# Kernel tuning notes

Measured on AMD Instinct MI355X. Metric: run time of the kernel, lower is better.

Reference implementation:

```python
import jax, jax.numpy as jnp
import numpy as np

D_MODEL = 1024
N_HEAD = 16
DK = D_MODEL // N_HEAD
D_FF = 2048
EPS = 1e-6
NEG = -1e10


def layer_norm(x, gamma, beta):
    # torch .std() is unbiased (N-1), and eps is added to std (not var)
    mean = jnp.mean(x, axis=-1, keepdims=True)
    var = jnp.sum((x - mean) ** 2, axis=-1, keepdims=True) / (x.shape[-1] - 1)
    std = jnp.sqrt(var)
    return gamma * (x - mean) / (std + EPS) + beta


def setup_inputs() -> dict:
    key = jax.random.key(0)
    ks = jax.random.split(key, 12)
    s = 0.02
    inp = {
        'x': jax.random.normal(ks[0], (16, 512, D_MODEL), dtype=jnp.float32),
        'x_mask': jax.random.randint(ks[1], (16, 1, 1, 512), 0, 2, dtype=jnp.int32),
        'Wq': jax.random.normal(ks[2], (D_MODEL, D_MODEL), dtype=jnp.float32) * s,
        'bq': jnp.zeros((D_MODEL,), jnp.float32),
        'Wk': jax.random.normal(ks[3], (D_MODEL, D_MODEL), dtype=jnp.float32) * s,
        'bk': jnp.zeros((D_MODEL,), jnp.float32),
        'Wv': jax.random.normal(ks[4], (D_MODEL, D_MODEL), dtype=jnp.float32) * s,
        'bv': jnp.zeros((D_MODEL,), jnp.float32),
        'Wo': jax.random.normal(ks[5], (D_MODEL, D_MODEL), dtype=jnp.float32) * s,
        'bo': jnp.zeros((D_MODEL,), jnp.float32),
        'gamma1': jnp.ones((D_MODEL,), jnp.float32),
        'beta1': jnp.zeros((D_MODEL,), jnp.float32),
        'W1': jax.random.normal(ks[6], (D_MODEL, D_FF), dtype=jnp.float32) * s,
        'b1': jnp.zeros((D_FF,), jnp.float32),
        'W2': jax.random.normal(ks[7], (D_FF, D_MODEL), dtype=jnp.float32) * s,
        'b2': jnp.zeros((D_MODEL,), jnp.float32),
        'gamma2': jnp.ones((D_MODEL,), jnp.float32),
        'beta2': jnp.zeros((D_MODEL,), jnp.float32),
    }
    return inp


def reference(x, x_mask, Wq, bq, Wk, bk, Wv, bv, Wo, bo, gamma1, beta1,
              W1, b1, W2, b2, gamma2, beta2):
    B, S, _ = x.shape
    # QKV projections -> [B, S, H, DK]
    q = (x @ Wq + bq).reshape(B, S, N_HEAD, DK)
    k = (x @ Wk + bk).reshape(B, S, N_HEAD, DK)
    v = (x @ Wv + bv).reshape(B, S, N_HEAD, DK)
    # scores [B, H, Sq, Sk]
    scores = jnp.einsum('bqhd,bkhd->bhqk', q, k) / jnp.sqrt(jnp.float32(DK))
    scores = jnp.where(x_mask == 0, jnp.float32(NEG), scores)
    probs = jax.nn.softmax(scores, axis=-1)
    attn = jnp.einsum('bhqk,bkhd->bqhd', probs, v).reshape(B, S, D_MODEL)
    attn_out = attn @ Wo + bo
    # residual + post-LN 1
    h = layer_norm(attn_out + x, gamma1, beta1)
    # FFN (exact GELU as torch nn.GELU default)
    ffn = jax.nn.gelu(h @ W1 + b1, approximate=False) @ W2 + b2
    out = layer_norm(ffn + h, gamma2, beta2)
    return out
```

## Files before the change

### kernel.cpp

```cpp
#include <hip/hip_runtime.h>
#include <math.h>

#define B_ 16
#define S_ 512
#define DM 1024
#define NH 16
#define DFF 2048

typedef short bf16x8 __attribute__((ext_vector_type(8)));
typedef float f32x4 __attribute__((ext_vector_type(4)));
typedef unsigned short u16;

__device__ __forceinline__ u16 f2bf(float f) {
  unsigned int u = __float_as_uint(f);
  u += 0x7FFF + ((u >> 16) & 1);
  return (u16)(u >> 16);
}

__device__ __forceinline__ float gelu_exact(float x) {
  return 0.5f * x * (1.0f + erff(x * 0.70710678118654752f));
}

__device__ __forceinline__ void gload_lds16(const void* g, void* l) {
  __builtin_amdgcn_global_load_lds((const __attribute__((address_space(1))) void*)g,
                                   (__attribute__((address_space(3))) void*)l, 16, 0, 0);
}


__global__ void cvt_bf16_k(const float* __restrict__ in, u16* __restrict__ out, int n) {
  int i = (blockIdx.x * blockDim.x + threadIdx.x) * 4;
  float4 v = *(const float4*)(in + i);
  uint2 pk;
  pk.x = (unsigned)f2bf(v.x) | ((unsigned)f2bf(v.y) << 16);
  pk.y = (unsigned)f2bf(v.z) | ((unsigned)f2bf(v.w) << 16);
  *(uint2*)(out + i) = pk;
}

__global__ void transpose_bf16(const float* __restrict__ W, u16* __restrict__ Wt, int K, int N) {
  __shared__ float tile[32][33];
  int n0 = blockIdx.x * 32, k0 = blockIdx.y * 32;
  int tx = threadIdx.x, ty = threadIdx.y;
#pragma unroll
  for (int j = 0; j < 32; j += 8)
    tile[ty + j][tx] = W[(size_t)(k0 + ty + j) * N + n0 + tx];
  __syncthreads();
#pragma unroll
  for (int j = 0; j < 32; j += 8)
    Wt[(size_t)(n0 + ty + j) * K + k0 + tx] = f2bf(tile[tx][ty + j]);
}

__global__ void bias_cat(const float* __restrict__ bq, const float* __restrict__ bk,
                         const float* __restrict__ bv, float* __restrict__ o) {
  int i = blockIdx.x * 256 + threadIdx.x;
  o[i] = (i < 1024) ? bq[i] : ((i < 2048) ? bk[i - 1024] : bv[i - 2048]);
}

template <int EPI>
__global__ __launch_bounds__(256, 3)
void gemm128(const u16* __restrict__ A, const u16* __restrict__ Bt,
             const float* __restrict__ bias, void* __restrict__ Cout,
             u16* __restrict__ vT, int M, int N, int K) {
  __shared__ __align__(16) char lds[65536];
  const int tid = threadIdx.x;
  const int w = tid >> 6, lane = tid & 63;
  const int wm = w >> 1, wn = w & 1;

  const int gx = gridDim.x;
  const int nwg = gx * gridDim.y;
  const int lin = blockIdx.y * gx + blockIdx.x;
  const int wg = (lin & 7) * (nwg >> 3) + (lin >> 3);
  const int bm = wg / gx, bn = wg % gx;

  const int NT = K >> 5;

  const int srow = tid >> 2;
  const int scol = ((tid & 3) * 8) ^ (((tid >> 5) & 1) * 16);
  const u16* gA = A + (size_t)(bm * 128 + srow) * K + scol;
  const u16* gB = Bt + (size_t)(bn * 128 + srow) * K + scol;
  const size_t rstep = (size_t)64 * K;
  char* const ldsA = lds;
  char* const ldsB = lds + 8192;
  const int dstbase = w * 1024;

  const int lr = lane & 15;
  const int kph = ((lane >> 4) * 16) ^ ((lane & 8) ? 32 : 0);
  const char* const fA = ldsA + (wm * 64 + lr) * 64 + kph;
  const char* const fB = ldsB + (wn * 64 + lr) * 64 + kph;

  f32x4 acc[4][4];
#pragma unroll
  for (int i = 0; i < 4; ++i)
#pragma unroll
    for (int j = 0; j < 4; ++j) acc[i][j] = (f32x4){0.f, 0.f, 0.f, 0.f};

#define STAGE_TILE(st_, slot_)                                     \
  do {                                                             \
    const u16* ga_ = gA + (st_) * 32;                              \
    const u16* gb_ = gB + (st_) * 32;                              \
    const int so_ = (slot_) * 16384;                               \
    gload_lds16(ga_, ldsA + so_ + dstbase);                        \
    gload_lds16(ga_ + rstep, ldsA + so_ + 4096 + dstbase);         \
    gload_lds16(gb_, ldsB + so_ + dstbase);                        \
    gload_lds16(gb_ + rstep, ldsB + so_ + 4096 + dstbase);         \
  } while (0)

  STAGE_TILE(0, 0);
  STAGE_TILE(1, 1);
  STAGE_TILE(2, 2);
  asm volatile("s_waitcnt vmcnt(4)" ::: "memory");
  __builtin_amdgcn_s_barrier();
  __builtin_amdgcn_sched_barrier(0);

  bf16x8 afP[4], bfP[4], afQ[4], bfQ[4];
  {
    const char* fAc = fA;
    const char* fBc = fB;
#pragma unroll
    for (int mi = 0; mi < 4; ++mi) afP[mi] = *(const bf16x8*)(fAc + mi * 1024);
#pragma unroll
    for (int ni = 0; ni < 4; ++ni) bfP[ni] = *(const bf16x8*)(fBc + ni * 1024);
  }
  asm volatile("s_waitcnt lgkmcnt(0)" ::: "memory");
  __builtin_amdgcn_sched_barrier(0);

  for (int tt = 0; tt < (NT >> 1); ++tt) {
    const int t = tt * 2;
    {
      const int rs = (t + 1) & 3;
      const char* fAc = fA + rs * 16384;
      const char* fBc = fB + rs * 16384;
#pragma unroll
      for (int mi = 0; mi < 4; ++mi) afQ[mi] = *(const bf16x8*)(fAc + mi * 1024);
#pragma unroll
      for (int ni = 0; ni < 4; ++ni) bfQ[ni] = *(const bf16x8*)(fBc + ni * 1024);
      const int st = (t + 3 < NT) ? (t + 3) : (NT - 1);
      STAGE_TILE(st, (t + 3) & 3);
      __builtin_amdgcn_s_setprio(1);
#pragma unroll
      for (int mi = 0; mi < 4; ++mi)
#pragma unroll
        for (int ni = 0; ni < 4; ++ni)
          acc[mi][ni] = __builtin_amdgcn_mfma_f32_16x16x32_bf16(afP[mi], bfP[ni], acc[mi][ni], 0, 0, 0);
      __builtin_amdgcn_s_setprio(0);
      asm volatile("s_waitcnt vmcnt(4) lgkmcnt(0)" ::: "memory");
      __builtin_amdgcn_s_barrier();
      __builtin_amdgcn_sched_barrier(0);
    }
    {
      const int rt = (t + 2 < NT) ? (t + 2) : (NT - 1);
      const int rs = rt & 3;
      const char* fAc = fA + rs * 16384;
      const char* fBc = fB + rs * 16384;
#pragma unroll
      for (int mi = 0; mi < 4; ++mi) afP[mi] = *(const bf16x8*)(fAc + mi * 1024);
#pragma unroll
      for (int ni = 0; ni < 4; ++ni) bfP[ni] = *(const bf16x8*)(fBc + ni * 1024);
      const int st = (t + 4 < NT) ? (t + 4) : (NT - 1);
      STAGE_TILE(st, (t + 4) & 3);
      __builtin_amdgcn_s_setprio(1);
#pragma unroll
      for (int mi = 0; mi < 4; ++mi)
#pragma unroll
        for (int ni = 0; ni < 4; ++ni)
          acc[mi][ni] = __builtin_amdgcn_mfma_f32_16x16x32_bf16(afQ[mi], bfQ[ni], acc[mi][ni], 0, 0, 0);
      __builtin_amdgcn_s_setprio(0);
      asm volatile("s_waitcnt vmcnt(4) lgkmcnt(0)" ::: "memory");
      __builtin_amdgcn_s_barrier();
      __builtin_amdgcn_sched_barrier(0);
    }
  }
#undef STAGE_TILE

  const int crow0 = bm * 128 + wm * 64;
  const int ccol0 = bn * 128 + wn * 64;
#pragma unroll
  for (int mi = 0; mi < 4; ++mi) {
#pragma unroll
    for (int ni = 0; ni < 4; ++ni) {
      const int col = ccol0 + ni * 16 + lr;
      const float bv = bias[col];
      const int rowb = crow0 + mi * 16 + (lane >> 4) * 4;
      float v[4];
#pragma unroll
      for (int r = 0; r < 4; ++r) v[r] = acc[mi][ni][r] + bv;
      if (EPI == 1) {
#pragma unroll
        for (int r = 0; r < 4; ++r)
          ((u16*)Cout)[(size_t)(rowb + r) * N + col] = f2bf(gelu_exact(v[r]));
      } else if (EPI == 2) {
#pragma unroll
        for (int r = 0; r < 4; ++r)
          ((float*)Cout)[(size_t)(rowb + r) * N + col] = v[r];
      } else {
        if (col < 2048) {
#pragma unroll
          for (int r = 0; r < 4; ++r)
            ((u16*)Cout)[(size_t)(rowb + r) * 2048 + col] = f2bf(v[r]);
        } else {
          const int b = rowb >> 9, s = rowb & 511;
          const int hd = col - 2048;
          ushort4 pk;
          pk.x = f2bf(v[0]); pk.y = f2bf(v[1]); pk.z = f2bf(v[2]); pk.w = f2bf(v[3]);
          *(ushort4*)(vT + ((size_t)(b * NH + (hd >> 6)) * 64 + (hd & 63)) * S_ + s) = pk;
        }
      }
    }
  }
}

__global__ __launch_bounds__(256, 3)
void attn_kernel(const u16* __restrict__ qk,
                 const u16* __restrict__ vT,
                 const int* __restrict__ mask,
                 u16* __restrict__ out) {
  __shared__ __align__(16) u16 Qs[32 * 72];
  __shared__ __align__(16) u16 Pl[32 * 520];
  __shared__ int Ml[512];
  __shared__ __align__(16) float Rmax[32][4];
  __shared__ __align__(16) float Rsum[32][4];

  const int tid = threadIdx.x;
  const int w = tid >> 6, lane = tid & 63;
  const int bid = blockIdx.x;
  const int widx = (bid & 7) * 512 + (bid >> 3);
  const int qt = widx & 15, h = (widx >> 4) & 15, b = widx >> 8;
  const int q0 = qt * 32;
  const int arow = lane & 15, kg = lane >> 4;

  {
    int r = tid >> 3, slot = tid & 7;
    bf16x8 v = *(const bf16x8*)(qk + (size_t)(b * S_ + q0 + r) * 2048 + h * 64 + slot * 8);
    *(bf16x8*)((char*)Qs + r * 144 + slot * 16) = v;
  }
  Ml[tid] = mask[b * S_ + tid];
  Ml[tid + 256] = mask[b * S_ + tid + 256];
  __syncthreads();

  f32x4 s0[8], s1[8];
  {
    bf16x8 af[2][2];
#pragma unroll
    for (int mi = 0; mi < 2; ++mi)
#pragma unroll
      for (int kk = 0; kk < 2; ++kk)
        af[mi][kk] = *(const bf16x8*)((char*)Qs + (mi * 16 + arow) * 144 + kk * 64 + kg * 16);
    const u16* kbase = qk + (size_t)(b * S_) * 2048 + 1024 + h * 64;
#pragma unroll
    for (int ni = 0; ni < 8; ++ni) {
      const int colg = w * 128 + ni * 16 + arow;
      const u16* kr = kbase + (size_t)colg * 2048 + kg * 8;
      bf16x8 bk0 = *(const bf16x8*)(kr);
      bf16x8 bk1 = *(const bf16x8*)(kr + 32);
      f32x4 a0 = {0.f, 0.f, 0.f, 0.f}, a1 = {0.f, 0.f, 0.f, 0.f};
      a0 = __builtin_amdgcn_mfma_f32_16x16x32_bf16(af[0][0], bk0, a0, 0, 0, 0);
      a0 = __builtin_amdgcn_mfma_f32_16x16x32_bf16(af[0][1], bk1, a0, 0, 0, 0);
      a1 = __builtin_amdgcn_mfma_f32_16x16x32_bf16(af[1][0], bk0, a1, 0, 0, 0);
      a1 = __builtin_amdgcn_mfma_f32_16x16x32_bf16(af[1][1], bk1, a1, 0, 0, 0);
      const bool msk = (Ml[colg] == 0);
#pragma unroll
      for (int r = 0; r < 4; ++r) {
        s0[ni][r] = msk ? -1e10f : a0[r] * 0.125f;
        s1[ni][r] = msk ? -1e10f : a1[r] * 0.125f;
      }
    }
  }

  float m0[4], m1[4];
#pragma unroll
  for (int r = 0; r < 4; ++r) {
    float a = fmaxf(fmaxf(s0[0][r], s0[1][r]), fmaxf(s0[2][r], s0[3][r]));
    float c = fmaxf(fmaxf(s0[4][r], s0[5][r]), fmaxf(s0[6][r], s0[7][r]));
    m0[r] = fmaxf(a, c);
    a = fmaxf(fmaxf(s1[0][r], s1[1][r]), fmaxf(s1[2][r], s1[3][r]));
    c = fmaxf(fmaxf(s1[4][r], s1[5][r]), fmaxf(s1[6][r], s1[7][r]));
    m1[r] = fmaxf(a, c);
  }
#pragma unroll
  for (int d = 1; d < 16; d <<= 1) {
#pragma unroll
    for (int r = 0; r < 4; ++r) {
      m0[r] = fmaxf(m0[r], __shfl_xor(m0[r], d));
      m1[r] = fmaxf(m1[r], __shfl_xor(m1[r], d));
    }
  }
  if (arow == 0) {
#pragma unroll
    for (int r = 0; r < 4; ++r) {
      Rmax[kg * 4 + r][w] = m0[r];
      Rmax[16 + kg * 4 + r][w] = m1[r];
    }
  }
  __syncthreads();
  float fm0[4], fm1[4];
#pragma unroll
  for (int r = 0; r < 4; ++r) {
    f32x4 v = *(const f32x4*)&Rmax[kg * 4 + r][0];
    fm0[r] = fmaxf(fmaxf(v[0], v[1]), fmaxf(v[2], v[3]));
    v = *(const f32x4*)&Rmax[16 + kg * 4 + r][0];
    fm1[r] = fmaxf(fmaxf(v[0], v[1]), fmaxf(v[2], v[3]));
  }

  float t0[4] = {0.f, 0.f, 0.f, 0.f}, t1[4] = {0.f, 0.f, 0.f, 0.f};
#pragma unroll
  for (int ni = 0; ni < 8; ++ni) {
#pragma unroll
    for (int r = 0; r < 4; ++r) {
      s0[ni][r] = __expf(s0[ni][r] - fm0[r]);
      t0[r] += s0[ni][r];
      s1[ni][r] = __expf(s1[ni][r] - fm1[r]);
      t1[r] += s1[ni][r];
    }
  }
#pragma unroll
  for (int ni = 0; ni < 8; ++ni) {
    const int colg = w * 128 + ni * 16 + arow;
#pragma unroll
    for (int r = 0; r < 4; ++r) {
      Pl[(kg * 4 + r) * 520 + colg] = f2bf(s0[ni][r]);
      Pl[(16 + kg * 4 + r) * 520 + colg] = f2bf(s1[ni][r]);
    }
  }
#pragma unroll
  for (int d = 1; d < 16; d <<= 1) {
#pragma unroll
    for (int r = 0; r < 4; ++r) {
      t0[r] += __shfl_xor(t0[r], d);
      t1[r] += __shfl_xor(t1[r], d);
    }
  }
  if (arow == 0) {
#pragma unroll
    for (int r = 0; r < 4; ++r) {
      Rsum[kg * 4 + r][w] = t0[r];
      Rsum[16 + kg * 4 + r][w] = t1[r];
    }
  }
  __syncthreads();

  {
    f32x4 oa[2];
    oa[0] = (f32x4){0.f, 0.f, 0.f, 0.f};
    oa[1] = (f32x4){0.f, 0.f, 0.f, 0.f};
    const u16* vb = vT + ((size_t)(b * NH + h) * 64 + w * 16 + arow) * S_ + kg * 8;
#pragma unroll
    for (int t16 = 0; t16 < 16; ++t16) {
      const int sk0 = t16 * 32;
      bf16x8 bfr = *(const bf16x8*)(vb + sk0);
#pragma unroll
      for (int mi = 0; mi < 2; ++mi) {
        bf16x8 pa = *(const bf16x8*)(Pl + (mi * 16 + arow) * 520 + sk0 + kg * 8);
        oa[mi] = __builtin_amdgcn_mfma_f32_16x16x32_bf16(pa, bfr, oa[mi], 0, 0, 0);
      }
    }
#pragma unroll
    for (int mi = 0; mi < 2; ++mi)
#pragma unroll
      for (int r = 0; r < 4; ++r) {
        const int rloc = mi * 16 + kg * 4 + r;
        f32x4 sv = *(const f32x4*)&Rsum[rloc][0];
        const float inv = 1.0f / (sv[0] + sv[1] + sv[2] + sv[3]);
        const int qrow = q0 + rloc;
        out[(size_t)(b * S_ + qrow) * DM + h * 64 + w * 16 + arow] = f2bf(oa[mi][r] * inv);
      }
  }
}

__global__ __launch_bounds__(256)
void ln_kernel(const float* __restrict__ a, const float* __restrict__ res,
               const float* __restrict__ gamma, const float* __restrict__ beta,
               float* __restrict__ out, u16* __restrict__ outb) {
  const int row = blockIdx.x, tid = threadIdx.x;
  const int w = tid >> 6, lane = tid & 63;
  const size_t base = (size_t)row * DM + tid * 4;
  float4 va = *(const float4*)(a + base);
  float4 vr = *(const float4*)(res + base);
  float v0 = va.x + vr.x, v1 = va.y + vr.y, v2 = va.z + vr.z, v3 = va.w + vr.w;
  float s = v0 + v1 + v2 + v3;
  float ss = v0 * v0 + v1 * v1 + v2 * v2 + v3 * v3;
#pragma unroll
  for (int off = 32; off >= 1; off >>= 1) {
    s += __shfl_down(s, off);
    ss += __shfl_down(ss, off);
  }
  __shared__ float ps[4], pss[4], mb[2];
  if (lane == 0) { ps[w] = s; pss[w] = ss; }
  __syncthreads();
  if (tid == 0) {
    float S = ps[0] + ps[1] + ps[2] + ps[3];
    float SS = pss[0] + pss[1] + pss[2] + pss[3];
    float mean = S * (1.0f / DM);
    float var = (SS - (float)DM * mean * mean) * (1.0f / (DM - 1));
    var = fmaxf(var, 0.f);
    mb[0] = mean;
    mb[1] = 1.0f / (sqrtf(var) + 1e-6f);
  }
  __syncthreads();
  const float mean = mb[0], rinv = mb[1];
  const int c = tid * 4;
  float y0 = gamma[c] * (v0 - mean) * rinv + beta[c];
  float y1 = gamma[c + 1] * (v1 - mean) * rinv + beta[c + 1];
  float y2 = gamma[c + 2] * (v2 - mean) * rinv + beta[c + 2];
  float y3 = gamma[c + 3] * (v3 - mean) * rinv + beta[c + 3];
  float4 o = {y0, y1, y2, y3};
  *(float4*)(out + base) = o;
  if (outb) {
    uint2 pk;
    pk.x = (unsigned)f2bf(y0) | ((unsigned)f2bf(y1) << 16);
    pk.y = (unsigned)f2bf(y2) | ((unsigned)f2bf(y3) << 16);
    *(uint2*)(outb + base) = pk;
  }
}


extern "C" void kernel_launch(void* const* d_in, const int* in_sizes, int n_in,
                              void* d_out, int out_size, void* d_ws, size_t ws_size,
                              hipStream_t stream) {
  const float* x = (const float*)d_in[0];
  const int* xm = (const int*)d_in[1];
  const float* Wq = (const float*)d_in[2];
  const float* bq = (const float*)d_in[3];
  const float* Wk = (const float*)d_in[4];
  const float* bk = (const float*)d_in[5];
  const float* Wv = (const float*)d_in[6];
  const float* bv = (const float*)d_in[7];
  const float* Wo = (const float*)d_in[8];
  const float* bo = (const float*)d_in[9];
  const float* g1 = (const float*)d_in[10];
  const float* be1 = (const float*)d_in[11];
  const float* W1 = (const float*)d_in[12];
  const float* b1 = (const float*)d_in[13];
  const float* W2 = (const float*)d_in[14];
  const float* b2 = (const float*)d_in[15];
  const float* g2 = (const float*)d_in[16];
  const float* be2 = (const float*)d_in[17];

  char* ws = (char*)d_ws;
  u16* xb = (u16*)(ws);
  u16* wqkvt = (u16*)(ws + 16777216);
  u16* wot = (u16*)(ws + 23068672);
  u16* w1t = (u16*)(ws + 25165824);
  u16* w2t = (u16*)(ws + 29360128);
  float* bqkv = (float*)(ws + 33554432);
  u16* qkb = (u16*)(ws + 33566720);
  u16* vtb = (u16*)(ws + 67121152);
  u16* attnb = (u16*)(ws + 83898368);
  float* f32a = (float*)(ws + 100675584);
  float* hbuf = (float*)(ws + 134230016);
  u16* hb = xb;

  cvt_bf16_k<<<dim3(8192), dim3(256), 0, stream>>>(x, xb, 8388608);
  transpose_bf16<<<dim3(32, 32), dim3(32, 8), 0, stream>>>(Wq, wqkvt, 1024, 1024);
  transpose_bf16<<<dim3(32, 32), dim3(32, 8), 0, stream>>>(Wk, wqkvt + 1024 * 1024, 1024, 1024);
  transpose_bf16<<<dim3(32, 32), dim3(32, 8), 0, stream>>>(Wv, wqkvt + 2 * 1024 * 1024, 1024, 1024);
  transpose_bf16<<<dim3(32, 32), dim3(32, 8), 0, stream>>>(Wo, wot, 1024, 1024);
  transpose_bf16<<<dim3(64, 32), dim3(32, 8), 0, stream>>>(W1, w1t, 1024, 2048);
  transpose_bf16<<<dim3(32, 64), dim3(32, 8), 0, stream>>>(W2, w2t, 2048, 1024);
  bias_cat<<<dim3(12), dim3(256), 0, stream>>>(bq, bk, bv, bqkv);

  gemm128<3><<<dim3(24, 64), dim3(256), 0, stream>>>(xb, wqkvt, bqkv, (void*)qkb, vtb, 8192, 3072, 1024);
  attn_kernel<<<dim3(4096), dim3(256), 0, stream>>>(qkb, vtb, xm, attnb);
  gemm128<2><<<dim3(8, 64), dim3(256), 0, stream>>>(attnb, wot, bo, (void*)f32a, (u16*)nullptr, 8192, 1024, 1024);
  ln_kernel<<<dim3(8192), dim3(256), 0, stream>>>(f32a, x, g1, be1, hbuf, hb);
  gemm128<1><<<dim3(16, 64), dim3(256), 0, stream>>>(hb, w1t, b1, (void*)qkb, (u16*)nullptr, 8192, 2048, 1024);
  gemm128<2><<<dim3(8, 64), dim3(256), 0, stream>>>(qkb, w2t, b2, (void*)f32a, (u16*)nullptr, 8192, 1024, 2048);
  ln_kernel<<<dim3(8192), dim3(256), 0, stream>>>(f32a, hbuf, g2, be2, (float*)d_out, (u16*)nullptr);
}
```

Baseline: 338.7 us.

## Enlarge GEMM tile to 256x128 with three-stage split A-half pipeline

The bf16 MFMA GEMM goes from 128x128 to 256x128 output tiles, so each wave holds 8x4 accumulators and each B fragment is reused across twice as many rows. The K-loop becomes a three-slot LDS ring (72KB), and each K step is split into two halves with staged A and B loads interleaved. The LDS swizzle changes to match. The aim is to cut global and LDS traffic per FLOP, at the cost of more registers and lower occupancy (launch bounds 2), half as many workgroups on the grid, and extra barriers per iteration.

```diff
diff --git a/kernel.cpp b/kernel.cpp
--- a/kernel.cpp
+++ b/kernel.cpp
@@ -56,11 +56,11 @@
 }
 
 template <int EPI>
-__global__ __launch_bounds__(256, 3)
-void gemm128(const u16* __restrict__ A, const u16* __restrict__ Bt,
-             const float* __restrict__ bias, void* __restrict__ Cout,
-             u16* __restrict__ vT, int M, int N, int K) {
-  __shared__ __align__(16) char lds[65536];
+__global__ __launch_bounds__(256, 2)
+void gemm_mfma(const u16* __restrict__ A, const u16* __restrict__ Bt,
+               const float* __restrict__ bias, void* __restrict__ Cout,
+               u16* __restrict__ vT, int M, int N, int K) {
+  __shared__ __align__(16) char lds[73728];
   const int tid = threadIdx.x;
   const int w = tid >> 6, lane = tid & 63;
   const int wm = w >> 1, wn = w & 1;
@@ -73,108 +73,98 @@
 
   const int NT = K >> 5;
 
-  const int srow = tid >> 2;
-  const int scol = ((tid & 3) * 8) ^ (((tid >> 5) & 1) * 16);
-  const u16* gA = A + (size_t)(bm * 128 + srow) * K + scol;
-  const u16* gB = Bt + (size_t)(bn * 128 + srow) * K + scol;
-  const size_t rstep = (size_t)64 * K;
-  char* const ldsA = lds;
-  char* const ldsB = lds + 8192;
-  const int dstbase = w * 1024;
-
-  const int lr = lane & 15;
-  const int kph = ((lane >> 4) * 16) ^ ((lane & 8) ? 32 : 0);
-  const char* const fA = ldsA + (wm * 64 + lr) * 64 + kph;
-  const char* const fB = ldsB + (wn * 64 + lr) * 64 + kph;
-
-  f32x4 acc[4][4];
-#pragma unroll
-  for (int i = 0; i < 4; ++i)
+  const int srow = w * 16 + (lane >> 2);
+  const int skel = ((lane & 3) ^ (lane >> 4)) * 8;
+  const u16* gA = A + (size_t)(bm * 256 + srow) * K + skel;
+  const u16* gB = Bt + (size_t)(bn * 128 + srow) * K + skel;
+  const size_t rs64 = (size_t)64 * K;
+  const int dstb = w * 1024;
+
+  const int lr = lane & 15, kg = lane >> 4;
+  const int kslot = (kg ^ ((lr >> 2) & 3)) << 4;
+  const int fAoff = (wm * 128 + lr) * 64 + kslot;
+  const int fBoff = 16384 + (wn * 64 + lr) * 64 + kslot;
+
+  f32x4 acc[8][4];
+#pragma unroll
+  for (int i = 0; i < 8; ++i)
 #pragma unroll
     for (int j = 0; j < 4; ++j) acc[i][j] = (f32x4){0.f, 0.f, 0.f, 0.f};
 
-#define STAGE_TILE(st_, slot_)                                     \
-  do {                                                             \
-    const u16* ga_ = gA + (st_) * 32;                              \
-    const u16* gb_ = gB + (st_) * 32;                              \
-    const int so_ = (slot_) * 16384;                               \
-    gload_lds16(ga_, ldsA + so_ + dstbase);                        \
-    gload_lds16(ga_ + rstep, ldsA + so_ + 4096 + dstbase);         \
-    gload_lds16(gb_, ldsB + so_ + dstbase);                        \
-    gload_lds16(gb_ + rstep, ldsB + so_ + 4096 + dstbase);         \
+#define STAGE_A(t_, sl_)                                         \
+  do {                                                           \
+    const u16* g_ = gA + (size_t)(t_) * 32;                      \
+    char* d_ = lds + (sl_) * 24576 + dstb;                       \
+    gload_lds16(g_, d_);                                         \
+    gload_lds16(g_ + rs64, d_ + 4096);                           \
+    gload_lds16(g_ + 2 * rs64, d_ + 8192);                       \
+    gload_lds16(g_ + 3 * rs64, d_ + 12288);                      \
   } while (0)
-
-  STAGE_TILE(0, 0);
-  STAGE_TILE(1, 1);
-  STAGE_TILE(2, 2);
-  asm volatile("s_waitcnt vmcnt(4)" ::: "memory");
+#define STAGE_B(t_, sl_)                                         \
+  do {                                                           \
+    const u16* g_ = gB + (size_t)(t_) * 32;                      \
+    char* d_ = lds + (sl_) * 24576 + 16384 + dstb;               \
+    gload_lds16(g_, d_);                                         \
+    gload_lds16(g_ + rs64, d_ + 4096);                           \
+  } while (0)
+
+  STAGE_A(0, 0);
+  STAGE_B(0, 0);
+  STAGE_A(1, 1);
+  STAGE_B(1, 1);
+  asm volatile("s_waitcnt vmcnt(6)" ::: "memory");
   __builtin_amdgcn_s_barrier();
   __builtin_amdgcn_sched_barrier(0);
 
-  bf16x8 afP[4], bfP[4], afQ[4], bfQ[4];
-  {
-    const char* fAc = fA;
-    const char* fBc = fB;
-#pragma unroll
-    for (int mi = 0; mi < 4; ++mi) afP[mi] = *(const bf16x8*)(fAc + mi * 1024);
-#pragma unroll
-    for (int ni = 0; ni < 4; ++ni) bfP[ni] = *(const bf16x8*)(fBc + ni * 1024);
-  }
-  asm volatile("s_waitcnt lgkmcnt(0)" ::: "memory");
-  __builtin_amdgcn_sched_barrier(0);
-
-  for (int tt = 0; tt < (NT >> 1); ++tt) {
-    const int t = tt * 2;
-    {
-      const int rs = (t + 1) & 3;
-      const char* fAc = fA + rs * 16384;
-      const char* fBc = fB + rs * 16384;
-#pragma unroll
-      for (int mi = 0; mi < 4; ++mi) afQ[mi] = *(const bf16x8*)(fAc + mi * 1024);
-#pragma unroll
-      for (int ni = 0; ni < 4; ++ni) bfQ[ni] = *(const bf16x8*)(fBc + ni * 1024);
-      const int st = (t + 3 < NT) ? (t + 3) : (NT - 1);
-      STAGE_TILE(st, (t + 3) & 3);
-      __builtin_amdgcn_s_setprio(1);
-#pragma unroll
-      for (int mi = 0; mi < 4; ++mi)
-#pragma unroll
-        for (int ni = 0; ni < 4; ++ni)
-          acc[mi][ni] = __builtin_amdgcn_mfma_f32_16x16x32_bf16(afP[mi], bfP[ni], acc[mi][ni], 0, 0, 0);
-      __builtin_amdgcn_s_setprio(0);
-      asm volatile("s_waitcnt vmcnt(4) lgkmcnt(0)" ::: "memory");
-      __builtin_amdgcn_s_barrier();
-      __builtin_amdgcn_sched_barrier(0);
-    }
-    {
-      const int rt = (t + 2 < NT) ? (t + 2) : (NT - 1);
-      const int rs = rt & 3;
-      const char* fAc = fA + rs * 16384;
-      const char* fBc = fB + rs * 16384;
-#pragma unroll
-      for (int mi = 0; mi < 4; ++mi) afP[mi] = *(const bf16x8*)(fAc + mi * 1024);
-#pragma unroll
-      for (int ni = 0; ni < 4; ++ni) bfP[ni] = *(const bf16x8*)(fBc + ni * 1024);
-      const int st = (t + 4 < NT) ? (t + 4) : (NT - 1);
-      STAGE_TILE(st, (t + 4) & 3);
-      __builtin_amdgcn_s_setprio(1);
-#pragma unroll
-      for (int mi = 0; mi < 4; ++mi)
-#pragma unroll
-        for (int ni = 0; ni < 4; ++ni)
-          acc[mi][ni] = __builtin_amdgcn_mfma_f32_16x16x32_bf16(afQ[mi], bfQ[ni], acc[mi][ni], 0, 0, 0);
-      __builtin_amdgcn_s_setprio(0);
-      asm volatile("s_waitcnt vmcnt(4) lgkmcnt(0)" ::: "memory");
-      __builtin_amdgcn_s_barrier();
-      __builtin_amdgcn_sched_barrier(0);
-    }
-  }
-#undef STAGE_TILE
-
-  const int crow0 = bm * 128 + wm * 64;
+  int cs = 0, ss = 2;
+  for (int t = 0; t < NT; ++t) {
+    const int st = (t + 2 < NT) ? (t + 2) : (NT - 1);
+    const char* fA = lds + cs * 24576 + fAoff;
+    const char* fB = lds + cs * 24576 + fBoff;
+    bf16x8 av[4], bv[4];
+#pragma unroll
+    for (int mi = 0; mi < 4; ++mi) av[mi] = *(const bf16x8*)(fA + mi * 1024);
+#pragma unroll
+    for (int ni = 0; ni < 4; ++ni) bv[ni] = *(const bf16x8*)(fB + ni * 1024);
+    STAGE_A(st, ss);
+    __builtin_amdgcn_s_barrier();
+    asm volatile("s_waitcnt lgkmcnt(0)" ::: "memory");
+    __builtin_amdgcn_sched_barrier(0);
+    __builtin_amdgcn_s_setprio(1);
+#pragma unroll
+    for (int mi = 0; mi < 4; ++mi)
+#pragma unroll
+      for (int ni = 0; ni < 4; ++ni)
+        acc[mi][ni] = __builtin_amdgcn_mfma_f32_16x16x32_bf16(av[mi], bv[ni], acc[mi][ni], 0, 0, 0);
+    __builtin_amdgcn_s_setprio(0);
+    __builtin_amdgcn_s_barrier();
+    __builtin_amdgcn_sched_barrier(0);
+#pragma unroll
+    for (int mi = 0; mi < 4; ++mi) av[mi] = *(const bf16x8*)(fA + 4096 + mi * 1024);
+    STAGE_B(st, ss);
+    __builtin_amdgcn_s_barrier();
+    asm volatile("s_waitcnt lgkmcnt(0)" ::: "memory");
+    __builtin_amdgcn_sched_barrier(0);
+    __builtin_amdgcn_s_setprio(1);
+#pragma unroll
+    for (int mi = 0; mi < 4; ++mi)
+#pragma unroll
+      for (int ni = 0; ni < 4; ++ni)
+        acc[4 + mi][ni] = __builtin_amdgcn_mfma_f32_16x16x32_bf16(av[mi], bv[ni], acc[4 + mi][ni], 0, 0, 0);
+    __builtin_amdgcn_s_setprio(0);
+    asm volatile("s_waitcnt vmcnt(6)" ::: "memory");
+    __builtin_amdgcn_s_barrier();
+    __builtin_amdgcn_sched_barrier(0);
+    cs = (cs == 2) ? 0 : cs + 1;
+    ss = (ss == 2) ? 0 : ss + 1;
+  }
+#undef STAGE_A
+#undef STAGE_B
+
+  const int crow0 = bm * 256 + wm * 128;
   const int ccol0 = bn * 128 + wn * 64;
 #pragma unroll
-  for (int mi = 0; mi < 4; ++mi) {
+  for (int mi = 0; mi < 8; ++mi) {
 #pragma unroll
     for (int ni = 0; ni < 4; ++ni) {
       const int col = ccol0 + ni * 16 + lr;
@@ -457,11 +447,11 @@
   transpose_bf16<<<dim3(32, 64), dim3(32, 8), 0, stream>>>(W2, w2t, 2048, 1024);
   bias_cat<<<dim3(12), dim3(256), 0, stream>>>(bq, bk, bv, bqkv);
 
-  gemm128<3><<<dim3(24, 64), dim3(256), 0, stream>>>(xb, wqkvt, bqkv, (void*)qkb, vtb, 8192, 3072, 1024);
+  gemm_mfma<3><<<dim3(24, 32), dim3(256), 0, stream>>>(xb, wqkvt, bqkv, (void*)qkb, vtb, 8192, 3072, 1024);
   attn_kernel<<<dim3(4096), dim3(256), 0, stream>>>(qkb, vtb, xm, attnb);
-  gemm128<2><<<dim3(8, 64), dim3(256), 0, stream>>>(attnb, wot, bo, (void*)f32a, (u16*)nullptr, 8192, 1024, 1024);
+  gemm_mfma<2><<<dim3(8, 32), dim3(256), 0, stream>>>(attnb, wot, bo, (void*)f32a, (u16*)nullptr, 8192, 1024, 1024);
   ln_kernel<<<dim3(8192), dim3(256), 0, stream>>>(f32a, x, g1, be1, hbuf, hb);
-  gemm128<1><<<dim3(16, 64), dim3(256), 0, stream>>>(hb, w1t, b1, (void*)qkb, (u16*)nullptr, 8192, 2048, 1024);
-  gemm128<2><<<dim3(8, 64), dim3(256), 0, stream>>>(qkb, w2t, b2, (void*)f32a, (u16*)nullptr, 8192, 1024, 2048);
+  gemm_mfma<1><<<dim3(16, 32), dim3(256), 0, stream>>>(hb, w1t, b1, (void*)qkb, (u16*)nullptr, 8192, 2048, 1024);
+  gemm_mfma<2><<<dim3(8, 32), dim3(256), 0, stream>>>(qkb, w2t, b2, (void*)f32a, (u16*)nullptr, 8192, 1024, 2048);
   ln_kernel<<<dim3(8192), dim3(256), 0, stream>>>(f32a, hbuf, g2, be2, (float*)d_out, (u16*)nullptr);
 }
```

After: 322.8 us. 4.7% less time.
